# Kernel optimization log

Hardware: AMD Instinct MI355X
Metric: run time of the kernel (lower is better)

## Reference

```python
import jax, jax.numpy as jnp
import numpy as np

N = 100000   # nodes
E = 1600000  # edges
F_IN = 256   # input features
H = 64       # hidden
C = 40       # classes


def setup_inputs() -> dict:
    key = jax.random.key(0)
    k = jax.random.split(key, 5)
    x = jax.random.normal(k[0], (N, F_IN), dtype=jnp.float32)
    edge_index = jax.random.randint(k[1], (2, E), 0, N, dtype=jnp.int64)
    edge_attr = jax.random.uniform(k[2], (E,), dtype=jnp.float32)
    # GCNConv params (glorot-ish scale), biases zero like reset_parameters
    W1 = jax.random.normal(k[3], (F_IN, H), dtype=jnp.float32) * (1.0 / np.sqrt(F_IN))
    b1 = jnp.zeros((H,), dtype=jnp.float32)
    W2 = jax.random.normal(k[4], (H, C), dtype=jnp.float32) * (1.0 / np.sqrt(H))
    b2 = jnp.zeros((C,), dtype=jnp.float32)
    return {"x": x, "edge_index": edge_index, "edge_attr": edge_attr,
            "W1": W1, "b1": b1, "W2": W2, "b2": b2}


def _gcn_conv(x, W, b, src, dst, norm):
    h = x @ W                                   # [N, out]
    msg = h[src] * norm[:, None]                # gather + edge scale [E+N, out]
    out = jax.ops.segment_sum(msg, dst, num_segments=N)
    return out + b


def reference(x, edge_index, edge_attr, W1, b1, W2, b2):
    # gcn_norm: add self-loops (weight 1), symmetric D^-1/2 A D^-1/2
    loop = jnp.arange(N, dtype=edge_index.dtype)
    src = jnp.concatenate([edge_index[0], loop])
    dst = jnp.concatenate([edge_index[1], loop])
    w = jnp.concatenate([edge_attr, jnp.ones((N,), dtype=edge_attr.dtype)])
    deg = jax.ops.segment_sum(w, dst, num_segments=N)
    dinv = jnp.where(deg > 0, jax.lax.rsqrt(jnp.maximum(deg, 1e-30)), 0.0)
    norm = dinv[src] * w * dinv[dst]

    h = _gcn_conv(x, W1, b1, src, dst, norm)
    h = jax.nn.relu(h)                          # dropout is identity in eval mode
    h = _gcn_conv(h, W2, b2, src, dst, norm)
    return jax.nn.log_softmax(h, axis=1)
```

## Files before the change

kernel.cpp:

```cpp
#include <hip/hip_runtime.h>
#include <math.h>

#define NN   100000
#define NE   1600000
#define FIN  256
#define HID  64
#define NC   40
#define NBKT 391
#define EPB  6250
#define CAP  4608

typedef __attribute__((ext_vector_type(8))) short short8;
typedef __attribute__((ext_vector_type(4))) float float4v;

static __device__ __forceinline__ short f2bf(float f) {
    unsigned u = __float_as_uint(f);
    u += 0x7FFFu + ((u >> 16) & 1u);
    return (short)(u >> 16);
}
static __device__ __forceinline__ float bf2f(unsigned short b) {
    return __uint_as_float((unsigned)b << 16);
}

__global__ __launch_bounds__(256) void w1cvt_k(const float* __restrict__ W1,
                                               short* __restrict__ w1t) {
    int t = blockIdx.x * 256 + threadIdx.x;
    int k = t >> 6, n = t & 63;
    w1t[n * FIN + k] = f2bf(W1[k * HID + n]);
}

__global__ __launch_bounds__(256) void phaseA_k(const int* __restrict__ src,
                                                const int* __restrict__ dst,
                                                const float* __restrict__ w,
                                                int* __restrict__ cursor,
                                                int2* __restrict__ bucketbuf) {
    __shared__ int  hist[NBKT];
    __shared__ int  sc[512];
    __shared__ int  loc_base[NBKT];
    __shared__ int  loc_cur[NBKT];
    __shared__ int  gb[NBKT];
    __shared__ int2 buf[EPB];
    const int t  = threadIdx.x;
    const int e0 = blockIdx.x * EPB;

    for (int i = t; i < NBKT; i += 256) hist[i] = 0;
    __syncthreads();
    for (int i = t; i < EPB; i += 256) atomicAdd(&hist[dst[e0 + i] >> 8], 1);
    __syncthreads();
    sc[t]       = (t       < NBKT) ? hist[t]       : 0;
    sc[t + 256] = (t + 256 < NBKT) ? hist[t + 256] : 0;
    __syncthreads();
    for (int off = 1; off < 512; off <<= 1) {
        int a0 = (t >= off) ? sc[t - off] : 0;
        int a1 = sc[t + 256 - off];
        __syncthreads();
        sc[t] += a0; sc[t + 256] += a1;
        __syncthreads();
    }
    for (int i = t; i < NBKT; i += 256) {
        int base = sc[i] - hist[i];
        loc_base[i] = base;
        loc_cur[i]  = base;
        gb[i] = atomicAdd(&cursor[i * 16], hist[i]);
    }
    __syncthreads();
    for (int i = t; i < EPB; i += 256) {
        int e = e0 + i;
        int d = dst[e];
        int b = d >> 8;
        int p = atomicAdd(&loc_cur[b], 1);
        buf[p] = make_int2(src[e] | ((d & 255) << 17), __float_as_int(w[e]));
    }
    __syncthreads();
    for (int b = t; b < NBKT; b += 256) {
        int lb = loc_base[b], n = hist[b];
        int2* dstp = bucketbuf + (size_t)b * CAP + gb[b];
        for (int i = 0; i < n; ++i) dstp[i] = buf[lb + i];
    }
}

__global__ __launch_bounds__(512) void scanB_k(const int* __restrict__ cursor,
                                               int* __restrict__ bucketbase,
                                               int* __restrict__ row_start) {
    __shared__ int tmp[512];
    int t = threadIdx.x;
    int v = (t < NBKT) ? cursor[t * 16] : 0;
    tmp[t] = v;
    __syncthreads();
    for (int off = 1; off < 512; off <<= 1) {
        int add = (t >= off) ? tmp[t - off] : 0;
        __syncthreads(); tmp[t] += add; __syncthreads();
    }
    if (t < NBKT) bucketbase[t] = tmp[t] - v;
    if (t == 0) { bucketbase[NBKT] = NE; row_start[NN] = NE; }
}

__global__ __launch_bounds__(256) void phaseB_k(const int* __restrict__ bucketbase,
                                                const int2* __restrict__ bucketbuf,
                                                int2* __restrict__ e8,
                                                int* __restrict__ row_start,
                                                float* __restrict__ dinv) {
    __shared__ int2 buf[CAP];
    __shared__ int2 buf2[CAP];
    __shared__ int  hist2[256];
    __shared__ int  tmp[256];
    __shared__ int  base2[257];
    __shared__ int  cur2[256];
    const int b = blockIdx.x, t = threadIdx.x;
    const int g0   = bucketbase[b];
    const int cntb = bucketbase[b + 1] - g0;
    const int n0   = b * 256;
    const int nnb  = (NN - n0 < 256) ? (NN - n0) : 256;

    hist2[t] = 0;
    __syncthreads();
    const int2* bb = bucketbuf + (size_t)b * CAP;
    for (int i = t; i < cntb; i += 256) {
        int2 kv = bb[i];
        buf[i] = kv;
        atomicAdd(&hist2[kv.x >> 17], 1);
    }
    __syncthreads();
    int v = hist2[t];
    tmp[t] = v;
    __syncthreads();
    for (int off = 1; off < 256; off <<= 1) {
        int add = (t >= off) ? tmp[t - off] : 0;
        __syncthreads(); tmp[t] += add; __syncthreads();
    }
    int excl = tmp[t] - v;
    base2[t] = excl;
    cur2[t]  = excl;
    if (t == 0) base2[256] = cntb;
    if (t < nnb) row_start[n0 + t] = g0 + excl;
    __syncthreads();
    for (int i = t; i < cntb; i += 256) {
        int2 kv = buf[i];
        int d = kv.x >> 17;
        int p = atomicAdd(&cur2[d], 1);
        buf2[p] = make_int2(kv.x & 0x1FFFF, kv.y);
    }
    __syncthreads();
    for (int i = t; i < cntb; i += 256) e8[g0 + i] = buf2[i];
    if (t < nnb) {
        float s = 0.f;
        int j1 = base2[t + 1];
        for (int j = base2[t]; j < j1; ++j) s += __int_as_float(buf2[j].y);
        dinv[n0 + t] = rsqrtf(1.0f + s);
    }
}

__global__ __launch_bounds__(256) void gemm1_mfma_k(const float* __restrict__ x,
                                                    const short* __restrict__ w1t,
                                                    const float* __restrict__ dinv,
                                                    unsigned short* __restrict__ h1) {
    __shared__ float xs[64 * 256];
    const int wave = threadIdx.x >> 6;
    const int lane = threadIdx.x & 63;
    const int m    = lane & 15;
    const int quad = lane >> 4;
    const int r0   = blockIdx.x * 64 + wave * 16;

    float* ldsrow0 = xs + (wave * 16) * 256;
#pragma unroll
    for (int j = 0; j < 16; ++j) {
        int rr  = r0 + j;
        int rcl = (rr < NN) ? rr : (NN - 1);
        const float* gsrc = x + (size_t)rcl * FIN + ((lane ^ (j & 7)) << 2);
        __builtin_amdgcn_global_load_lds(
            (const __attribute__((address_space(1))) void*)gsrc,
            (__attribute__((address_space(3))) void*)(ldsrow0 + j * 256),
            16, 0, 0);
    }
    asm volatile("s_waitcnt vmcnt(0)" ::: "memory");

    const char* xrow = (const char*)(xs + (wave * 16 + m) * 256);
    const unsigned sw = (unsigned)(m & 7) << 4;

    float4v acc0 = {0.f,0.f,0.f,0.f}, acc1 = acc0, acc2 = acc0, acc3 = acc0;

#pragma unroll
    for (int kc = 0; kc < 8; ++kc) {
        const int kof = kc * 32 + quad * 8;
        const unsigned c0 = (unsigned)(kc * 128 + quad * 32);
        float4v xa = *(const float4v*)(xrow + (c0 ^ sw));
        float4v xb = *(const float4v*)(xrow + ((c0 + 16) ^ sw));
        short8 a;
        a[0] = f2bf(xa[0]); a[1] = f2bf(xa[1]); a[2] = f2bf(xa[2]); a[3] = f2bf(xa[3]);
        a[4] = f2bf(xb[0]); a[5] = f2bf(xb[1]); a[6] = f2bf(xb[2]); a[7] = f2bf(xb[3]);
        short8 b0 = *(const short8*)(w1t + (0 * 16 + m) * FIN + kof);
        short8 b1 = *(const short8*)(w1t + (1 * 16 + m) * FIN + kof);
        short8 b2 = *(const short8*)(w1t + (2 * 16 + m) * FIN + kof);
        short8 b3 = *(const short8*)(w1t + (3 * 16 + m) * FIN + kof);
        acc0 = __builtin_amdgcn_mfma_f32_16x16x32_bf16(a, b0, acc0, 0, 0, 0);
        acc1 = __builtin_amdgcn_mfma_f32_16x16x32_bf16(a, b1, acc1, 0, 0, 0);
        acc2 = __builtin_amdgcn_mfma_f32_16x16x32_bf16(a, b2, acc2, 0, 0, 0);
        acc3 = __builtin_amdgcn_mfma_f32_16x16x32_bf16(a, b3, acc3, 0, 0, 0);
    }
#pragma unroll
    for (int r = 0; r < 4; ++r) {
        int rr = r0 + quad * 4 + r;
        if (rr < NN) {
            float dv = dinv[rr];
            unsigned short* hp = h1 + (size_t)rr * HID + m;
            hp[0]  = (unsigned short)f2bf(acc0[r] * dv);
            hp[16] = (unsigned short)f2bf(acc1[r] * dv);
            hp[32] = (unsigned short)f2bf(acc2[r] * dv);
            hp[48] = (unsigned short)f2bf(acc3[r] * dv);
        }
    }
}

__global__ __launch_bounds__(256) void gatherA_k(const int* __restrict__ row_start,
                                                 const int2* __restrict__ e8,
                                                 const float* __restrict__ dinv,
                                                 const unsigned short* __restrict__ h,
                                                 const float* __restrict__ b1,
                                                 unsigned short* __restrict__ Rp) {
    const int v    = blockIdx.x * 4 + (threadIdx.x >> 6);
    const int lane = threadIdx.x & 63;
    const int slot = lane >> 3;
    const int fg   = lane & 7;
    const int i0 = row_start[v], i1 = row_start[v + 1];

    float acc[8] = {0.f,0.f,0.f,0.f,0.f,0.f,0.f,0.f};
    for (int i = i0; i < i1; i += 16) {
        int iiA = i + slot, iiB = i + 8 + slot;
        bool okA = iiA < i1, okB = iiB < i1;
        int2 eA = e8[okA ? iiA : (NE - 1)];
        int2 eB = e8[okB ? iiB : (NE - 1)];
        int  sA = okA ? eA.x : 0;
        int  sB = okB ? eB.x : 0;
        float wA = okA ? __int_as_float(eA.y) : 0.f;
        float wB = okB ? __int_as_float(eB.y) : 0.f;
        uint4 pA = *(const uint4*)(h + (size_t)sA * HID + fg * 8);
        uint4 pB = *(const uint4*)(h + (size_t)sB * HID + fg * 8);
        acc[0] = fmaf(__uint_as_float(pA.x << 16),         wA, acc[0]);
        acc[1] = fmaf(__uint_as_float(pA.x & 0xFFFF0000u), wA, acc[1]);
        acc[2] = fmaf(__uint_as_float(pA.y << 16),         wA, acc[2]);
        acc[3] = fmaf(__uint_as_float(pA.y & 0xFFFF0000u), wA, acc[3]);
        acc[4] = fmaf(__uint_as_float(pA.z << 16),         wA, acc[4]);
        acc[5] = fmaf(__uint_as_float(pA.z & 0xFFFF0000u), wA, acc[5]);
        acc[6] = fmaf(__uint_as_float(pA.w << 16),         wA, acc[6]);
        acc[7] = fmaf(__uint_as_float(pA.w & 0xFFFF0000u), wA, acc[7]);
        acc[0] = fmaf(__uint_as_float(pB.x << 16),         wB, acc[0]);
        acc[1] = fmaf(__uint_as_float(pB.x & 0xFFFF0000u), wB, acc[1]);
        acc[2] = fmaf(__uint_as_float(pB.y << 16),         wB, acc[2]);
        acc[3] = fmaf(__uint_as_float(pB.y & 0xFFFF0000u), wB, acc[3]);
        acc[4] = fmaf(__uint_as_float(pB.z << 16),         wB, acc[4]);
        acc[5] = fmaf(__uint_as_float(pB.z & 0xFFFF0000u), wB, acc[5]);
        acc[6] = fmaf(__uint_as_float(pB.w << 16),         wB, acc[6]);
        acc[7] = fmaf(__uint_as_float(pB.w & 0xFFFF0000u), wB, acc[7]);
    }
#pragma unroll
    for (int mk = 8; mk <= 32; mk <<= 1) {
#pragma unroll
        for (int q = 0; q < 8; ++q) acc[q] += __shfl_xor(acc[q], mk);
    }

    const float dv = dinv[v];
    uint4 ps = *(const uint4*)(h + (size_t)v * HID + fg * 8);
    float4 bA = *(const float4*)(b1 + fg * 8);
    float4 bB = *(const float4*)(b1 + fg * 8 + 4);
    float r0 = fmaxf(dv * (acc[0] + __uint_as_float(ps.x << 16))         + bA.x, 0.f);
    float r1 = fmaxf(dv * (acc[1] + __uint_as_float(ps.x & 0xFFFF0000u)) + bA.y, 0.f);
    float r2 = fmaxf(dv * (acc[2] + __uint_as_float(ps.y << 16))         + bA.z, 0.f);
    float r3 = fmaxf(dv * (acc[3] + __uint_as_float(ps.y & 0xFFFF0000u)) + bA.w, 0.f);
    float r4 = fmaxf(dv * (acc[4] + __uint_as_float(ps.z << 16))         + bB.x, 0.f);
    float r5 = fmaxf(dv * (acc[5] + __uint_as_float(ps.z & 0xFFFF0000u)) + bB.y, 0.f);
    float r6 = fmaxf(dv * (acc[6] + __uint_as_float(ps.w << 16))         + bB.z, 0.f);
    float r7 = fmaxf(dv * (acc[7] + __uint_as_float(ps.w & 0xFFFF0000u)) + bB.w, 0.f);
    if (slot == 0) {
        uint4 pk;
        pk.x = (unsigned)(unsigned short)f2bf(dv * r0) | ((unsigned)(unsigned short)f2bf(dv * r1) << 16);
        pk.y = (unsigned)(unsigned short)f2bf(dv * r2) | ((unsigned)(unsigned short)f2bf(dv * r3) << 16);
        pk.z = (unsigned)(unsigned short)f2bf(dv * r4) | ((unsigned)(unsigned short)f2bf(dv * r5) << 16);
        pk.w = (unsigned)(unsigned short)f2bf(dv * r6) | ((unsigned)(unsigned short)f2bf(dv * r7) << 16);
        *(uint4*)(Rp + (size_t)v * HID + fg * 8) = pk;
    }
}

__global__ __launch_bounds__(256) void gatherB_k(const int* __restrict__ row_start,
                                                 const int2* __restrict__ e8,
                                                 const float* __restrict__ dinv,
                                                 const unsigned short* __restrict__ Rp,
                                                 float* __restrict__ agg2) {
    const int v    = blockIdx.x * 4 + (threadIdx.x >> 6);
    const int lane = threadIdx.x & 63;
    const int slot = lane >> 3;
    const int fg   = lane & 7;
    const int i0 = row_start[v], i1 = row_start[v + 1];

    float acc[8] = {0.f,0.f,0.f,0.f,0.f,0.f,0.f,0.f};
    for (int i = i0; i < i1; i += 16) {
        int iiA = i + slot, iiB = i + 8 + slot;
        bool okA = iiA < i1, okB = iiB < i1;
        int2 eA = e8[okA ? iiA : (NE - 1)];
        int2 eB = e8[okB ? iiB : (NE - 1)];
        int  sA = okA ? eA.x : 0;
        int  sB = okB ? eB.x : 0;
        float wA = okA ? __int_as_float(eA.y) : 0.f;
        float wB = okB ? __int_as_float(eB.y) : 0.f;
        uint4 pA = *(const uint4*)(Rp + (size_t)sA * HID + fg * 8);
        uint4 pB = *(const uint4*)(Rp + (size_t)sB * HID + fg * 8);
        acc[0] = fmaf(__uint_as_float(pA.x << 16),         wA, acc[0]);
        acc[1] = fmaf(__uint_as_float(pA.x & 0xFFFF0000u), wA, acc[1]);
        acc[2] = fmaf(__uint_as_float(pA.y << 16),         wA, acc[2]);
        acc[3] = fmaf(__uint_as_float(pA.y & 0xFFFF0000u), wA, acc[3]);
        acc[4] = fmaf(__uint_as_float(pA.z << 16),         wA, acc[4]);
        acc[5] = fmaf(__uint_as_float(pA.z & 0xFFFF0000u), wA, acc[5]);
        acc[6] = fmaf(__uint_as_float(pA.w << 16),         wA, acc[6]);
        acc[7] = fmaf(__uint_as_float(pA.w & 0xFFFF0000u), wA, acc[7]);
        acc[0] = fmaf(__uint_as_float(pB.x << 16),         wB, acc[0]);
        acc[1] = fmaf(__uint_as_float(pB.x & 0xFFFF0000u), wB, acc[1]);
        acc[2] = fmaf(__uint_as_float(pB.y << 16),         wB, acc[2]);
        acc[3] = fmaf(__uint_as_float(pB.y & 0xFFFF0000u), wB, acc[3]);
        acc[4] = fmaf(__uint_as_float(pB.z << 16),         wB, acc[4]);
        acc[5] = fmaf(__uint_as_float(pB.z & 0xFFFF0000u), wB, acc[5]);
        acc[6] = fmaf(__uint_as_float(pB.w << 16),         wB, acc[6]);
        acc[7] = fmaf(__uint_as_float(pB.w & 0xFFFF0000u), wB, acc[7]);
    }
#pragma unroll
    for (int mk = 8; mk <= 32; mk <<= 1) {
#pragma unroll
        for (int q = 0; q < 8; ++q) acc[q] += __shfl_xor(acc[q], mk);
    }

    const float dv = dinv[v];
    uint4 ps = *(const uint4*)(Rp + (size_t)v * HID + fg * 8);
    if (slot == 0) {
        float4 oA, oB;
        oA.x = dv * (acc[0] + __uint_as_float(ps.x << 16));
        oA.y = dv * (acc[1] + __uint_as_float(ps.x & 0xFFFF0000u));
        oA.z = dv * (acc[2] + __uint_as_float(ps.y << 16));
        oA.w = dv * (acc[3] + __uint_as_float(ps.y & 0xFFFF0000u));
        oB.x = dv * (acc[4] + __uint_as_float(ps.z << 16));
        oB.y = dv * (acc[5] + __uint_as_float(ps.z & 0xFFFF0000u));
        oB.z = dv * (acc[6] + __uint_as_float(ps.w << 16));
        oB.w = dv * (acc[7] + __uint_as_float(ps.w & 0xFFFF0000u));
        *(float4*)(agg2 + (size_t)v * HID + fg * 8)     = oA;
        *(float4*)(agg2 + (size_t)v * HID + fg * 8 + 4) = oB;
    }
}

__global__ __launch_bounds__(256) void gemm3_logsm_k(const float* __restrict__ agg2,
                                                     const float* __restrict__ W2,
                                                     const float* __restrict__ b2,
                                                     float* __restrict__ out) {
    __shared__ float w2s[HID * NC];
    __shared__ float b2s[NC];
    for (int i = threadIdx.x; i < HID * NC; i += 256) w2s[i] = W2[i];
    if (threadIdx.x < NC) b2s[threadIdx.x] = b2[threadIdx.x];
    __syncthreads();

    const int r = blockIdx.x * 256 + threadIdx.x;
    if (r >= NN) return;
    float acc[NC];
#pragma unroll
    for (int c = 0; c < NC; ++c) acc[c] = b2s[c];

    const float4* row4 = (const float4*)(agg2 + (size_t)r * HID);
    for (int kk = 0; kk < HID; kk += 4) {
        float4 v = row4[kk >> 2];
#pragma unroll
        for (int c = 0; c < NC; ++c) {
            acc[c] = fmaf(v.x, w2s[(kk + 0) * NC + c], acc[c]);
            acc[c] = fmaf(v.y, w2s[(kk + 1) * NC + c], acc[c]);
            acc[c] = fmaf(v.z, w2s[(kk + 2) * NC + c], acc[c]);
            acc[c] = fmaf(v.w, w2s[(kk + 3) * NC + c], acc[c]);
        }
    }
    float m = acc[0];
#pragma unroll
    for (int c = 1; c < NC; ++c) m = fmaxf(m, acc[c]);
    float s = 0.f;
#pragma unroll
    for (int c = 0; c < NC; ++c) s += __expf(acc[c] - m);
    float lg = m + __logf(s);
    float* outp = out + (size_t)r * NC;
#pragma unroll
    for (int c = 0; c < NC; c += 4)
        *(float4*)&outp[c] = make_float4(acc[c] - lg, acc[c+1] - lg, acc[c+2] - lg, acc[c+3] - lg);
}

extern "C" void kernel_launch(void* const* d_in, const int* in_sizes, int n_in,
                              void* d_out, int out_size, void* d_ws, size_t ws_size,
                              hipStream_t stream) {
    const float* x  = (const float*)d_in[0];
    const int*   ei = (const int*)d_in[1];
    const float* ea = (const float*)d_in[2];
    const float* W1 = (const float*)d_in[3];
    const float* b1 = (const float*)d_in[4];
    const float* W2 = (const float*)d_in[5];
    const float* b2 = (const float*)d_in[6];
    const int* src = ei;
    const int* dst = ei + NE;
    float* out = (float*)d_out;

    char* ws = (char*)d_ws;
    float* dinv       = (float*)(ws + 0);
    int*   row_start  = (int*)  (ws + 400000);
    int*   cursor     = (int*)  (ws + 800016);
    int*   bucketbase = (int*)  (ws + 825040);
    int2*  e8         = (int2*) (ws + 826608);
    unsigned short* h1 = (unsigned short*)(ws + 13626608);
    unsigned short* Rp = (unsigned short*)(ws + 26426608);
    float* agg2       = (float*)(ws + 39226608);
    short* w1t        = (short*)(ws + 64826608);
    int2*  bucketbuf  = (int2*)agg2;

    hipMemsetAsync(cursor, 0, 391 * 16 * sizeof(int), stream);

    w1cvt_k <<<64,   256, 0, stream>>>(W1, w1t);
    phaseA_k<<<256,  256, 0, stream>>>(src, dst, ea, cursor, bucketbuf);
    scanB_k <<<1,    512, 0, stream>>>(cursor, bucketbase, row_start);
    phaseB_k<<<NBKT, 256, 0, stream>>>(bucketbase, bucketbuf, e8, row_start, dinv);

    gemm1_mfma_k <<<(NN + 63) / 64, 256, 0, stream>>>(x, w1t, dinv, h1);
    gatherA_k    <<<NN / 4, 256, 0, stream>>>(row_start, e8, dinv, h1, b1, Rp);
    gatherB_k    <<<NN / 4, 256, 0, stream>>>(row_start, e8, dinv, Rp, agg2);
    gemm3_logsm_k<<<(NN + 255) / 256, 256, 0, stream>>>(agg2, W2, b2, out);
}
```

Baseline: 385.7 us.

## Make GEMM1 persistent with double-buffered LDS staging and fold dinv into edges

GEMM1 becomes a persistent kernel of 256 blocks. Each wave loops over 16-row tiles, keeps W1 fragments in registers and double-buffers the x tile in LDS with async global-to-LDS loads, so the load of the next tile overlaps the MFMA work on the current one. The source-side dinv factor moves out of h1 and into the edge weights through a new e8scale kernel. Both gather kernels compensate with a dv² term on the self-loop. This adds an extra pass over the 1.6M edges and gives GEMM1 high register pressure at one block per SM.

```diff
diff --git a/kernel.cpp b/kernel.cpp
--- a/kernel.cpp
+++ b/kernel.cpp
@@ -9,6 +9,7 @@
 #define NBKT 391
 #define EPB  6250
 #define CAP  4608
+#define NT   6250
 
 typedef __attribute__((ext_vector_type(8))) short short8;
 typedef __attribute__((ext_vector_type(4))) float float4v;
@@ -150,64 +151,85 @@
     }
 }
 
-__global__ __launch_bounds__(256) void gemm1_mfma_k(const float* __restrict__ x,
-                                                    const short* __restrict__ w1t,
-                                                    const float* __restrict__ dinv,
-                                                    unsigned short* __restrict__ h1) {
-    __shared__ float xs[64 * 256];
+__global__ __launch_bounds__(256) void e8scale_k(int2* __restrict__ e8,
+                                                 const float* __restrict__ dinv) {
+    int e = blockIdx.x * 256 + threadIdx.x;
+    int2 kv = e8[e];
+    kv.y = __float_as_int(__int_as_float(kv.y) * dinv[kv.x]);
+    e8[e] = kv;
+}
+
+static __device__ __forceinline__ void stage_tile(const float* __restrict__ x, int t,
+                                                  float* buf, int lane) {
+#pragma unroll
+    for (int j = 0; j < 16; ++j) {
+        const float* gsrc = x + (size_t)t * (16 * FIN) + j * FIN + ((lane ^ (j & 7)) << 2);
+        __builtin_amdgcn_global_load_lds(
+            (const __attribute__((address_space(1))) void*)gsrc,
+            (__attribute__((address_space(3))) void*)(buf + j * 256), 16, 0, 0);
+    }
+}
+
+__global__ __launch_bounds__(256, 1) void gemm1_mfma_k(const float* __restrict__ x,
+                                                       const short* __restrict__ w1t,
+                                                       unsigned short* __restrict__ h1) {
+    __shared__ float xs[4 * 2 * 16 * 256];
     const int wave = threadIdx.x >> 6;
     const int lane = threadIdx.x & 63;
     const int m    = lane & 15;
     const int quad = lane >> 4;
-    const int r0   = blockIdx.x * 64 + wave * 16;
-
-    float* ldsrow0 = xs + (wave * 16) * 256;
-#pragma unroll
-    for (int j = 0; j < 16; ++j) {
-        int rr  = r0 + j;
-        int rcl = (rr < NN) ? rr : (NN - 1);
-        const float* gsrc = x + (size_t)rcl * FIN + ((lane ^ (j & 7)) << 2);
-        __builtin_amdgcn_global_load_lds(
-            (const __attribute__((address_space(1))) void*)gsrc,
-            (__attribute__((address_space(3))) void*)(ldsrow0 + j * 256),
-            16, 0, 0);
-    }
-    asm volatile("s_waitcnt vmcnt(0)" ::: "memory");
-
-    const char* xrow = (const char*)(xs + (wave * 16 + m) * 256);
+    const int wid  = blockIdx.x * 4 + wave;
+
+    short8 bf[4][8];
+#pragma unroll
+    for (int nb = 0; nb < 4; ++nb)
+#pragma unroll
+        for (int kc = 0; kc < 8; ++kc)
+            bf[nb][kc] = *(const short8*)(w1t + (nb * 16 + m) * FIN + kc * 32 + quad * 8);
+
+    float* buf0 = xs + (wave * 2) * (16 * 256);
+    float* buf1 = buf0 + 16 * 256;
     const unsigned sw = (unsigned)(m & 7) << 4;
 
-    float4v acc0 = {0.f,0.f,0.f,0.f}, acc1 = acc0, acc2 = acc0, acc3 = acc0;
-
-#pragma unroll
-    for (int kc = 0; kc < 8; ++kc) {
-        const int kof = kc * 32 + quad * 8;
-        const unsigned c0 = (unsigned)(kc * 128 + quad * 32);
-        float4v xa = *(const float4v*)(xrow + (c0 ^ sw));
-        float4v xb = *(const float4v*)(xrow + ((c0 + 16) ^ sw));
-        short8 a;
-        a[0] = f2bf(xa[0]); a[1] = f2bf(xa[1]); a[2] = f2bf(xa[2]); a[3] = f2bf(xa[3]);
-        a[4] = f2bf(xb[0]); a[5] = f2bf(xb[1]); a[6] = f2bf(xb[2]); a[7] = f2bf(xb[3]);
-        short8 b0 = *(const short8*)(w1t + (0 * 16 + m) * FIN + kof);
-        short8 b1 = *(const short8*)(w1t + (1 * 16 + m) * FIN + kof);
-        short8 b2 = *(const short8*)(w1t + (2 * 16 + m) * FIN + kof);
-        short8 b3 = *(const short8*)(w1t + (3 * 16 + m) * FIN + kof);
-        acc0 = __builtin_amdgcn_mfma_f32_16x16x32_bf16(a, b0, acc0, 0, 0, 0);
-        acc1 = __builtin_amdgcn_mfma_f32_16x16x32_bf16(a, b1, acc1, 0, 0, 0);
-        acc2 = __builtin_amdgcn_mfma_f32_16x16x32_bf16(a, b2, acc2, 0, 0, 0);
-        acc3 = __builtin_amdgcn_mfma_f32_16x16x32_bf16(a, b3, acc3, 0, 0, 0);
-    }
-#pragma unroll
-    for (int r = 0; r < 4; ++r) {
-        int rr = r0 + quad * 4 + r;
-        if (rr < NN) {
-            float dv = dinv[rr];
+    int t = wid, cur = 0;
+    if (t < NT) stage_tile(x, t, buf0, lane);
+    for (; t < NT; t += 1024) {
+        int tn = t + 1024;
+        float* bcur  = cur ? buf1 : buf0;
+        float* bnext = cur ? buf0 : buf1;
+        if (tn < NT) {
+            stage_tile(x, tn, bnext, lane);
+            asm volatile("s_waitcnt vmcnt(16)" ::: "memory");
+        } else {
+            asm volatile("s_waitcnt vmcnt(0)" ::: "memory");
+        }
+        __builtin_amdgcn_sched_barrier(0);
+
+        const char* xrow = (const char*)(bcur + m * 256);
+        float4v acc0 = {0.f,0.f,0.f,0.f}, acc1 = acc0, acc2 = acc0, acc3 = acc0;
+#pragma unroll
+        for (int kc = 0; kc < 8; ++kc) {
+            const unsigned c0 = (unsigned)(kc * 128 + quad * 32);
+            float4v xa = *(const float4v*)(xrow + (c0 ^ sw));
+            float4v xb = *(const float4v*)(xrow + ((c0 + 16) ^ sw));
+            short8 a;
+            a[0] = f2bf(xa[0]); a[1] = f2bf(xa[1]); a[2] = f2bf(xa[2]); a[3] = f2bf(xa[3]);
+            a[4] = f2bf(xb[0]); a[5] = f2bf(xb[1]); a[6] = f2bf(xb[2]); a[7] = f2bf(xb[3]);
+            acc0 = __builtin_amdgcn_mfma_f32_16x16x32_bf16(a, bf[0][kc], acc0, 0, 0, 0);
+            acc1 = __builtin_amdgcn_mfma_f32_16x16x32_bf16(a, bf[1][kc], acc1, 0, 0, 0);
+            acc2 = __builtin_amdgcn_mfma_f32_16x16x32_bf16(a, bf[2][kc], acc2, 0, 0, 0);
+            acc3 = __builtin_amdgcn_mfma_f32_16x16x32_bf16(a, bf[3][kc], acc3, 0, 0, 0);
+        }
+#pragma unroll
+        for (int r = 0; r < 4; ++r) {
+            int rr = t * 16 + quad * 4 + r;
             unsigned short* hp = h1 + (size_t)rr * HID + m;
-            hp[0]  = (unsigned short)f2bf(acc0[r] * dv);
-            hp[16] = (unsigned short)f2bf(acc1[r] * dv);
-            hp[32] = (unsigned short)f2bf(acc2[r] * dv);
-            hp[48] = (unsigned short)f2bf(acc3[r] * dv);
+            hp[0]  = (unsigned short)f2bf(acc0[r]);
+            hp[16] = (unsigned short)f2bf(acc1[r]);
+            hp[32] = (unsigned short)f2bf(acc2[r]);
+            hp[48] = (unsigned short)f2bf(acc3[r]);
         }
+        cur ^= 1;
     }
 }
 
@@ -258,24 +280,25 @@
         for (int q = 0; q < 8; ++q) acc[q] += __shfl_xor(acc[q], mk);
     }
 
-    const float dv = dinv[v];
+    const float dv  = dinv[v];
+    const float dv2 = dv * dv;
     uint4 ps = *(const uint4*)(h + (size_t)v * HID + fg * 8);
     float4 bA = *(const float4*)(b1 + fg * 8);
     float4 bB = *(const float4*)(b1 + fg * 8 + 4);
-    float r0 = fmaxf(dv * (acc[0] + __uint_as_float(ps.x << 16))         + bA.x, 0.f);
-    float r1 = fmaxf(dv * (acc[1] + __uint_as_float(ps.x & 0xFFFF0000u)) + bA.y, 0.f);
-    float r2 = fmaxf(dv * (acc[2] + __uint_as_float(ps.y << 16))         + bA.z, 0.f);
-    float r3 = fmaxf(dv * (acc[3] + __uint_as_float(ps.y & 0xFFFF0000u)) + bA.w, 0.f);
-    float r4 = fmaxf(dv * (acc[4] + __uint_as_float(ps.z << 16))         + bB.x, 0.f);
-    float r5 = fmaxf(dv * (acc[5] + __uint_as_float(ps.z & 0xFFFF0000u)) + bB.y, 0.f);
-    float r6 = fmaxf(dv * (acc[6] + __uint_as_float(ps.w << 16))         + bB.z, 0.f);
-    float r7 = fmaxf(dv * (acc[7] + __uint_as_float(ps.w & 0xFFFF0000u)) + bB.w, 0.f);
+    float r0 = fmaxf(dv * acc[0] + dv2 * __uint_as_float(ps.x << 16)         + bA.x, 0.f);
+    float r1 = fmaxf(dv * acc[1] + dv2 * __uint_as_float(ps.x & 0xFFFF0000u) + bA.y, 0.f);
+    float r2 = fmaxf(dv * acc[2] + dv2 * __uint_as_float(ps.y << 16)         + bA.z, 0.f);
+    float r3 = fmaxf(dv * acc[3] + dv2 * __uint_as_float(ps.y & 0xFFFF0000u) + bA.w, 0.f);
+    float r4 = fmaxf(dv * acc[4] + dv2 * __uint_as_float(ps.z << 16)         + bB.x, 0.f);
+    float r5 = fmaxf(dv * acc[5] + dv2 * __uint_as_float(ps.z & 0xFFFF0000u) + bB.y, 0.f);
+    float r6 = fmaxf(dv * acc[6] + dv2 * __uint_as_float(ps.w << 16)         + bB.z, 0.f);
+    float r7 = fmaxf(dv * acc[7] + dv2 * __uint_as_float(ps.w & 0xFFFF0000u) + bB.w, 0.f);
     if (slot == 0) {
         uint4 pk;
-        pk.x = (unsigned)(unsigned short)f2bf(dv * r0) | ((unsigned)(unsigned short)f2bf(dv * r1) << 16);
-        pk.y = (unsigned)(unsigned short)f2bf(dv * r2) | ((unsigned)(unsigned short)f2bf(dv * r3) << 16);
-        pk.z = (unsigned)(unsigned short)f2bf(dv * r4) | ((unsigned)(unsigned short)f2bf(dv * r5) << 16);
-        pk.w = (unsigned)(unsigned short)f2bf(dv * r6) | ((unsigned)(unsigned short)f2bf(dv * r7) << 16);
+        pk.x = (unsigned)(unsigned short)f2bf(r0) | ((unsigned)(unsigned short)f2bf(r1) << 16);
+        pk.y = (unsigned)(unsigned short)f2bf(r2) | ((unsigned)(unsigned short)f2bf(r3) << 16);
+        pk.z = (unsigned)(unsigned short)f2bf(r4) | ((unsigned)(unsigned short)f2bf(r5) << 16);
+        pk.w = (unsigned)(unsigned short)f2bf(r6) | ((unsigned)(unsigned short)f2bf(r7) << 16);
         *(uint4*)(Rp + (size_t)v * HID + fg * 8) = pk;
     }
 }
@@ -326,18 +349,19 @@
         for (int q = 0; q < 8; ++q) acc[q] += __shfl_xor(acc[q], mk);
     }
 
-    const float dv = dinv[v];
+    const float dv  = dinv[v];
+    const float dv2 = dv * dv;
     uint4 ps = *(const uint4*)(Rp + (size_t)v * HID + fg * 8);
     if (slot == 0) {
         float4 oA, oB;
-        oA.x = dv * (acc[0] + __uint_as_float(ps.x << 16));
-        oA.y = dv * (acc[1] + __uint_as_float(ps.x & 0xFFFF0000u));
-        oA.z = dv * (acc[2] + __uint_as_float(ps.y << 16));
-        oA.w = dv * (acc[3] + __uint_as_float(ps.y & 0xFFFF0000u));
-        oB.x = dv * (acc[4] + __uint_as_float(ps.z << 16));
-        oB.y = dv * (acc[5] + __uint_as_float(ps.z & 0xFFFF0000u));
-        oB.z = dv * (acc[6] + __uint_as_float(ps.w << 16));
-        oB.w = dv * (acc[7] + __uint_as_float(ps.w & 0xFFFF0000u));
+        oA.x = dv * acc[0] + dv2 * __uint_as_float(ps.x << 16);
+        oA.y = dv * acc[1] + dv2 * __uint_as_float(ps.x & 0xFFFF0000u);
+        oA.z = dv * acc[2] + dv2 * __uint_as_float(ps.y << 16);
+        oA.w = dv * acc[3] + dv2 * __uint_as_float(ps.y & 0xFFFF0000u);
+        oB.x = dv * acc[4] + dv2 * __uint_as_float(ps.z << 16);
+        oB.y = dv * acc[5] + dv2 * __uint_as_float(ps.z & 0xFFFF0000u);
+        oB.z = dv * acc[6] + dv2 * __uint_as_float(ps.w << 16);
+        oB.w = dv * acc[7] + dv2 * __uint_as_float(ps.w & 0xFFFF0000u);
         *(float4*)(agg2 + (size_t)v * HID + fg * 8)     = oA;
         *(float4*)(agg2 + (size_t)v * HID + fg * 8 + 4) = oB;
     }
@@ -415,8 +439,9 @@
     phaseA_k<<<256,  256, 0, stream>>>(src, dst, ea, cursor, bucketbuf);
     scanB_k <<<1,    512, 0, stream>>>(cursor, bucketbase, row_start);
     phaseB_k<<<NBKT, 256, 0, stream>>>(bucketbase, bucketbuf, e8, row_start, dinv);
-
-    gemm1_mfma_k <<<(NN + 63) / 64, 256, 0, stream>>>(x, w1t, dinv, h1);
+    e8scale_k<<<NE / 256, 256, 0, stream>>>(e8, dinv);
+
+    gemm1_mfma_k <<<256,  256, 0, stream>>>(x, w1t, h1);
     gatherA_k    <<<NN / 4, 256, 0, stream>>>(row_start, e8, dinv, h1, b1, Rp);
     gatherB_k    <<<NN / 4, 256, 0, stream>>>(row_start, e8, dinv, Rp, agg2);
     gemm3_logsm_k<<<(NN + 255) / 256, 256, 0, stream>>>(agg2, W2, b2, out);
```

After: 378.1 us. -2.0%, faster.
